# Performance work log

Hardware: AMD Instinct MI355X
Metric: run time of the kernel (lower is better)

## Reference

```python
import jax, jax.numpy as jnp
import numpy as np

B = 2048
GIN = 128      # gating input features
GH = 128       # gating hidden units
E = 8          # experts
XIN = 512      # expert input features
U = 512        # expert layer units
OUT = 512      # expert output features


def setup_inputs() -> dict:
    key = jax.random.key(0)
    ks = jax.random.split(key, 16)
    rn = lambda k, shape: (jax.random.normal(k, shape) * 0.05).astype(jnp.float32)
    return {
        "gating_input": jax.random.normal(ks[0], (B, GIN), dtype=jnp.float32),
        "expert_input": jax.random.normal(ks[1], (B, XIN), dtype=jnp.float32),
        # gating MLP params (Dense stores kernel as (in, out))
        "Wg0": rn(ks[2], (GIN, GH)), "bg0": rn(ks[3], (GH,)),
        "Wg1": rn(ks[4], (GH, GH)), "bg1": rn(ks[5], (GH,)),
        "Wgo": rn(ks[6], (GH, E)),  "bgo": rn(ks[7], (E,)),
        # expert weight pools: alpha (E, units, in), beta (E, units)
        "alpha0": rn(ks[8], (E, U, XIN)), "beta0": rn(ks[9], (E, U)),
        "alpha1": rn(ks[10], (E, U, U)),  "beta1": rn(ks[11], (E, U)),
        "alpha2": rn(ks[12], (E, OUT, U)), "beta2": rn(ks[13], (E, OUT)),
    }


def dense_expert(x, g, alpha, beta):
    # Mathematically: (sum_e g[b,e] * alpha[e]) @ x[b] + sum_e g[b,e]*beta[e]
    # Contract input with each expert first (avoids the (B,U,I) blended-weight tensor).
    per_expert = jnp.einsum("bi,eui->beu", x, alpha)   # (B, E, U)
    w = jnp.einsum("be,beu->bu", g, per_expert)         # (B, U)
    b = jnp.einsum("be,eu->bu", g, beta)                # (B, U)
    return w + b


def reference(gating_input, expert_input, Wg0, bg0, Wg1, bg1, Wgo, bgo,
              alpha0, beta0, alpha1, beta1, alpha2, beta2):
    # Gating network: Dense+ELU x2 (dropout is identity at inference), Dense+softmax
    h = jax.nn.elu(gating_input @ Wg0 + bg0)
    h = jax.nn.elu(h @ Wg1 + bg1)
    g = jax.nn.softmax(h @ Wgo + bgo, axis=-1)          # (B, E)

    # Expert network: DenseExpert + ELU x2, final DenseExpert
    x = jax.nn.elu(dense_expert(expert_input, g, alpha0, beta0))
    x = jax.nn.elu(dense_expert(x, g, alpha1, beta1))
    y = dense_expert(x, g, alpha2, beta2)               # (B, OUT)
    return y
```

## Files before the change

kernel.cpp:

```cpp
#include <hip/hip_runtime.h>
#include <math.h>

#define BATCH 2048
#define GIN 128
#define GH 128
#define NE 8
#define XIN 512
#define UU 512
#define NPAIR 4

typedef __attribute__((ext_vector_type(8))) short short8;
typedef __attribute__((ext_vector_type(4))) float f32x4;

__device__ inline unsigned short f2bf(float f) {
    unsigned u = __float_as_uint(f);
    u += 0x7fffu + ((u >> 16) & 1u);
    return (unsigned short)(u >> 16);
}

__device__ inline float elu1(float x) { return x > 0.f ? x : (expf(x) - 1.f); }

__global__ __launch_bounds__(256) void gating_kernel(
    const float* __restrict__ gin, const float* __restrict__ W0, const float* __restrict__ b0,
    const float* __restrict__ W1, const float* __restrict__ b1,
    const float* __restrict__ Wo, const float* __restrict__ bo,
    float* __restrict__ g)
{
    __shared__ float xs[4][128];
    __shared__ float hs[4][128];
    __shared__ float ps[2][4][128];
    __shared__ float lp[8][4][8];
    __shared__ float ls[4][8];

    const int t = threadIdx.x;
    const int c = t & 127;
    const int h = t >> 7;
    const int row0 = blockIdx.x * 4;

    ((float*)xs)[t]       = gin[row0 * GIN + t];
    ((float*)xs)[t + 256] = gin[row0 * GIN + t + 256];
    __syncthreads();

    {
        float acc0 = 0.f, acc1 = 0.f, acc2 = 0.f, acc3 = 0.f;
        const float* Wc = W0 + c;
        #pragma unroll 8
        for (int i = h * 64; i < h * 64 + 64; ++i) {
            float w = Wc[i * GH];
            acc0 += xs[0][i] * w; acc1 += xs[1][i] * w;
            acc2 += xs[2][i] * w; acc3 += xs[3][i] * w;
        }
        ps[h][0][c] = acc0; ps[h][1][c] = acc1; ps[h][2][c] = acc2; ps[h][3][c] = acc3;
    }
    __syncthreads();
    {
        int o = t, r = o >> 7, cc = o & 127;
        hs[r][cc] = elu1(ps[0][r][cc] + ps[1][r][cc] + b0[cc]);
        o = t + 256; r = o >> 7; cc = o & 127;
        hs[r][cc] = elu1(ps[0][r][cc] + ps[1][r][cc] + b0[cc]);
    }
    __syncthreads();

    {
        float acc0 = 0.f, acc1 = 0.f, acc2 = 0.f, acc3 = 0.f;
        const float* Wc = W1 + c;
        #pragma unroll 8
        for (int i = h * 64; i < h * 64 + 64; ++i) {
            float w = Wc[i * GH];
            acc0 += hs[0][i] * w; acc1 += hs[1][i] * w;
            acc2 += hs[2][i] * w; acc3 += hs[3][i] * w;
        }
        ps[h][0][c] = acc0; ps[h][1][c] = acc1; ps[h][2][c] = acc2; ps[h][3][c] = acc3;
    }
    __syncthreads();
    {
        int o = t, r = o >> 7, cc = o & 127;
        xs[r][cc] = elu1(ps[0][r][cc] + ps[1][r][cc] + b1[cc]);
        o = t + 256; r = o >> 7; cc = o & 127;
        xs[r][cc] = elu1(ps[0][r][cc] + ps[1][r][cc] + b1[cc]);
    }
    __syncthreads();

    {
        const int e = t & 7, r = (t >> 3) & 3, q = t >> 5;
        float s = 0.f;
        #pragma unroll
        for (int i = q * 16; i < q * 16 + 16; ++i) s += xs[r][i] * Wo[i * NE + e];
        lp[q][r][e] = s;
    }
    __syncthreads();
    if (t < 32) {
        const int r = t >> 3, e = t & 7;
        float s = bo[e];
        #pragma unroll
        for (int q = 0; q < 8; ++q) s += lp[q][r][e];
        ls[r][e] = s;
    }
    __syncthreads();
    if (t < 4) {
        float mx = ls[t][0];
        #pragma unroll
        for (int e = 1; e < 8; ++e) mx = fmaxf(mx, ls[t][e]);
        float s = 0.f, ex[8];
        #pragma unroll
        for (int e = 0; e < 8; ++e) { ex[e] = expf(ls[t][e] - mx); s += ex[e]; }
        float inv = 1.f / s;
        #pragma unroll
        for (int e = 0; e < 8; ++e) g[(row0 + t) * NE + e] = ex[e] * inv;
    }
}

__global__ __launch_bounds__(256) void convert_alpha_kernel(
    const float* __restrict__ a0, const float* __restrict__ a1, const float* __restrict__ a2,
    unsigned short* __restrict__ ab)
{
    const long long vi = (long long)(blockIdx.x * blockDim.x + threadIdx.x) * 4;
    const int a = (int)(vi >> 21);
    const int off = (int)(vi & ((1 << 21) - 1));
    const float* src = (a == 0) ? a0 : ((a == 1) ? a1 : a2);
    float4 v = *(const float4*)(src + off);
    union { unsigned short us[4]; uint2 u2; } p;
    p.us[0] = f2bf(v.x); p.us[1] = f2bf(v.y); p.us[2] = f2bf(v.z); p.us[3] = f2bf(v.w);
    *(uint2*)(ab + vi) = p.u2;
}

__global__ __launch_bounds__(256) void xcast_kernel(
    const float* __restrict__ x, unsigned short* __restrict__ Xb)
{
    const int gid4 = (blockIdx.x * blockDim.x + threadIdx.x) * 4;
    const float4 v = *(const float4*)(x + gid4);
    union { unsigned short us[4]; uint2 u2; } p;
    p.us[0] = f2bf(v.x); p.us[1] = f2bf(v.y); p.us[2] = f2bf(v.z); p.us[3] = f2bf(v.w);
    *(uint2*)(Xb + gid4) = p.u2;
}

__global__ __launch_bounds__(256) void moe_gemm_kernel(
    const unsigned short* __restrict__ A,
    const unsigned short* __restrict__ Bw,
    const float* __restrict__ g,
    float* __restrict__ Cp)
{
    constexpr int M = BATCH, N = UU, K = XIN;
    __shared__ unsigned short As[128 * 64];
    __shared__ unsigned short Bs0[64 * 64];
    __shared__ unsigned short Bs1[64 * 64];
    __shared__ float gs[128][2];

    const int t = threadIdx.x;
    const int n0 = blockIdx.x * 64;
    const int m0 = blockIdx.y * 128;
    const int z = blockIdx.z;
    const int e0 = 2 * z, e1 = 2 * z + 1;
    const int wave = t >> 6, lane = t & 63;
    const int wm = (wave >> 1) * 64;
    const int wn = (wave & 1) * 32;

    if (t < 128) {
        gs[t][0] = g[(m0 + t) * NE + e0];
        gs[t][1] = g[(m0 + t) * NE + e1];
    }

    f32x4 acc0[4][2] = {};
    f32x4 acc1[4][2] = {};

    const int trow = t >> 3;
    const int tcol = (t & 7) * 8;

    const unsigned short* Ae  = A  + (size_t)m0 * K;
    const unsigned short* Be0 = Bw + ((size_t)e0 * N + n0) * K;
    const unsigned short* Be1 = Bw + ((size_t)e1 * N + n0) * K;

    for (int ki = 0; ki < K; ki += 64) {
        __syncthreads();
        #pragma unroll
        for (int it = 0; it < 4; ++it) {
            const unsigned short* ga = Ae + (size_t)(trow + it * 32) * K + ki + tcol;
            __builtin_amdgcn_global_load_lds(
                (const __attribute__((address_space(1))) void*)ga,
                (__attribute__((address_space(3))) void*)(As + it * 2048 + t * 8), 16, 0, 0);
        }
        #pragma unroll
        for (int it = 0; it < 2; ++it) {
            const unsigned short* gb0 = Be0 + (size_t)(trow + it * 32) * K + ki + tcol;
            __builtin_amdgcn_global_load_lds(
                (const __attribute__((address_space(1))) void*)gb0,
                (__attribute__((address_space(3))) void*)(Bs0 + it * 2048 + t * 8), 16, 0, 0);
            const unsigned short* gb1 = Be1 + (size_t)(trow + it * 32) * K + ki + tcol;
            __builtin_amdgcn_global_load_lds(
                (const __attribute__((address_space(1))) void*)gb1,
                (__attribute__((address_space(3))) void*)(Bs1 + it * 2048 + t * 8), 16, 0, 0);
        }
        __syncthreads();

        #pragma unroll
        for (int kk = 0; kk < 64; kk += 32) {
            short8 af[4], bf0[2], bf1[2];
            const int fr = lane & 15;
            const int fk = kk + (lane >> 4) * 8;
            #pragma unroll
            for (int i = 0; i < 4; ++i) af[i] = *(const short8*)(As + (wm + fr + i * 16) * 64 + fk);
            #pragma unroll
            for (int j = 0; j < 2; ++j) {
                bf0[j] = *(const short8*)(Bs0 + (wn + fr + j * 16) * 64 + fk);
                bf1[j] = *(const short8*)(Bs1 + (wn + fr + j * 16) * 64 + fk);
            }
            #pragma unroll
            for (int i = 0; i < 4; ++i)
                #pragma unroll
                for (int j = 0; j < 2; ++j) {
                    acc0[i][j] = __builtin_amdgcn_mfma_f32_16x16x32_bf16(af[i], bf0[j], acc0[i][j], 0, 0, 0);
                    acc1[i][j] = __builtin_amdgcn_mfma_f32_16x16x32_bf16(af[i], bf1[j], acc1[i][j], 0, 0, 0);
                }
        }
    }

    float* Cb = Cp + (size_t)z * M * N;
    const int cl = lane & 15, rq = lane >> 4;
    #pragma unroll
    for (int i = 0; i < 4; ++i)
        #pragma unroll
        for (int j = 0; j < 2; ++j)
            #pragma unroll
            for (int r = 0; r < 4; ++r) {
                const int rl = wm + i * 16 + rq * 4 + r;
                const int col = n0 + wn + j * 16 + cl;
                const float v = gs[rl][0] * acc0[i][j][r] + gs[rl][1] * acc1[i][j][r];
                Cb[(size_t)(m0 + rl) * N + col] = v;
            }
}

__global__ __launch_bounds__(256) void reduce_kernel(
    const float* __restrict__ Cp, const float* __restrict__ g,
    const float* __restrict__ beta, unsigned short* __restrict__ Xnext,
    float* __restrict__ out, int last)
{
    const int gid4 = (blockIdx.x * blockDim.x + threadIdx.x) * 4;
    const int b = gid4 >> 9, u = gid4 & 511;
    float4 v = {0.f, 0.f, 0.f, 0.f};
    #pragma unroll
    for (int s = 0; s < NPAIR; ++s) {
        float4 p = *(const float4*)(Cp + (size_t)s * (BATCH * (size_t)UU) + gid4);
        v.x += p.x; v.y += p.y; v.z += p.z; v.w += p.w;
    }
    const float* gb = g + b * NE;
    #pragma unroll
    for (int e = 0; e < NE; ++e) {
        const float ge = gb[e];
        float4 bb = *(const float4*)(beta + e * UU + u);
        v.x += ge * bb.x; v.y += ge * bb.y; v.z += ge * bb.z; v.w += ge * bb.w;
    }
    if (last) {
        *(float4*)(out + gid4) = v;
    } else {
        union { unsigned short us[4]; uint2 u2; } p;
        p.us[0] = f2bf(elu1(v.x)); p.us[1] = f2bf(elu1(v.y));
        p.us[2] = f2bf(elu1(v.z)); p.us[3] = f2bf(elu1(v.w));
        *(uint2*)(Xnext + gid4) = p.u2;
    }
}

extern "C" void kernel_launch(void* const* d_in, const int* in_sizes, int n_in,
                              void* d_out, int out_size, void* d_ws, size_t ws_size,
                              hipStream_t stream)
{
    (void)in_sizes; (void)n_in; (void)out_size; (void)ws_size;
    const float* gin = (const float*)d_in[0];
    const float* xin = (const float*)d_in[1];
    const float* W0  = (const float*)d_in[2];
    const float* b0  = (const float*)d_in[3];
    const float* W1  = (const float*)d_in[4];
    const float* b1  = (const float*)d_in[5];
    const float* Wo  = (const float*)d_in[6];
    const float* bo  = (const float*)d_in[7];
    const float* alpha[3] = {(const float*)d_in[8],  (const float*)d_in[10], (const float*)d_in[12]};
    const float* beta[3]  = {(const float*)d_in[9],  (const float*)d_in[11], (const float*)d_in[13]};
    float* out = (float*)d_out;

    char* ws = (char*)d_ws;
    float* g = (float*)ws;
    size_t off = 65536;
    unsigned short* ab = (unsigned short*)(ws + off);
    off += (size_t)3 * (1 << 21) * 2;
    unsigned short* Xb = (unsigned short*)(ws + off);
    off += (size_t)BATCH * XIN * 2;
    float* Cp = (float*)(ws + off);

    gating_kernel<<<BATCH / 4, 256, 0, stream>>>(gin, W0, b0, W1, b1, Wo, bo, g);
    convert_alpha_kernel<<<(3 * (1 << 21)) / 4 / 256, 256, 0, stream>>>(alpha[0], alpha[1], alpha[2], ab);
    xcast_kernel<<<(BATCH * XIN) / 4 / 256, 256, 0, stream>>>(xin, Xb);

    for (int l = 0; l < 3; ++l) {
        moe_gemm_kernel<<<dim3(UU / 64, BATCH / 128, NPAIR), 256, 0, stream>>>(
            Xb, ab + (size_t)l * (1 << 21), g, Cp);
        reduce_kernel<<<(BATCH * UU) / 4 / 256, 256, 0, stream>>>(
            Cp, g, beta[l], Xb, out, l == 2 ? 1 : 0);
    }
}
```

Baseline: 183.4 us.

## Fuse all-expert GEMM with gating reduction, bias and ELU epilogue

Each block now computes a 64x32 output tile for all 8 experts at once and folds gating weights, the bias mix and ELU into the epilogue. This removes the fp32 partial-sum buffer and the separate reduce kernel per layer. Ping-pong activation buffers are used, and the x cast is merged into the alpha conversion launch. The cost is more accumulator registers (16 f32x4 per wave), a smaller A tile with less reuse, and non-coalesced scalar stores in the epilogue.

Result: faster. 157.4 us (-14.2%).

```diff
diff --git a/kernel.cpp b/kernel.cpp
--- a/kernel.cpp
+++ b/kernel.cpp
@@ -7,7 +7,6 @@
 #define NE 8
 #define XIN 512
 #define UU 512
-#define NPAIR 4
 
 typedef __attribute__((ext_vector_type(8))) short short8;
 typedef __attribute__((ext_vector_type(4))) float f32x4;
@@ -110,153 +109,102 @@
     }
 }
 
-__global__ __launch_bounds__(256) void convert_alpha_kernel(
+__global__ __launch_bounds__(256) void convert_kernel(
     const float* __restrict__ a0, const float* __restrict__ a1, const float* __restrict__ a2,
-    unsigned short* __restrict__ ab)
+    const float* __restrict__ xv, unsigned short* __restrict__ dst)
 {
     const long long vi = (long long)(blockIdx.x * blockDim.x + threadIdx.x) * 4;
-    const int a = (int)(vi >> 21);
-    const int off = (int)(vi & ((1 << 21) - 1));
-    const float* src = (a == 0) ? a0 : ((a == 1) ? a1 : a2);
-    float4 v = *(const float4*)(src + off);
+    const int sel = (int)(vi >> 21);
+    const float* src = (sel == 0) ? a0 : (sel == 1) ? a1 : (sel == 2) ? a2 : xv;
+    float4 v = *(const float4*)(src + (vi & ((1 << 21) - 1)));
     union { unsigned short us[4]; uint2 u2; } p;
     p.us[0] = f2bf(v.x); p.us[1] = f2bf(v.y); p.us[2] = f2bf(v.z); p.us[3] = f2bf(v.w);
-    *(uint2*)(ab + vi) = p.u2;
-}
-
-__global__ __launch_bounds__(256) void xcast_kernel(
-    const float* __restrict__ x, unsigned short* __restrict__ Xb)
-{
-    const int gid4 = (blockIdx.x * blockDim.x + threadIdx.x) * 4;
-    const float4 v = *(const float4*)(x + gid4);
-    union { unsigned short us[4]; uint2 u2; } p;
-    p.us[0] = f2bf(v.x); p.us[1] = f2bf(v.y); p.us[2] = f2bf(v.z); p.us[3] = f2bf(v.w);
-    *(uint2*)(Xb + gid4) = p.u2;
-}
-
-__global__ __launch_bounds__(256) void moe_gemm_kernel(
+    *(uint2*)(dst + vi) = p.u2;
+}
+
+__global__ __launch_bounds__(256) void moe_fused_kernel(
     const unsigned short* __restrict__ A,
     const unsigned short* __restrict__ Bw,
     const float* __restrict__ g,
-    float* __restrict__ Cp)
-{
-    constexpr int M = BATCH, N = UU, K = XIN;
-    __shared__ unsigned short As[128 * 64];
-    __shared__ unsigned short Bs0[64 * 64];
-    __shared__ unsigned short Bs1[64 * 64];
-    __shared__ float gs[128][2];
+    const float* __restrict__ beta,
+    unsigned short* __restrict__ Xnext,
+    float* __restrict__ out, int last)
+{
+    constexpr int K = XIN;
+    __shared__ unsigned short As[64 * 64];
+    __shared__ unsigned short Bs[8 * 32 * 64];
+    __shared__ float gs[64][8];
+    __shared__ float bt[8][32];
 
     const int t = threadIdx.x;
-    const int n0 = blockIdx.x * 64;
-    const int m0 = blockIdx.y * 128;
-    const int z = blockIdx.z;
-    const int e0 = 2 * z, e1 = 2 * z + 1;
+    const int n0 = blockIdx.x * 32;
+    const int m0 = blockIdx.y * 64;
     const int wave = t >> 6, lane = t & 63;
-    const int wm = (wave >> 1) * 64;
-    const int wn = (wave & 1) * 32;
-
-    if (t < 128) {
-        gs[t][0] = g[(m0 + t) * NE + e0];
-        gs[t][1] = g[(m0 + t) * NE + e1];
-    }
-
-    f32x4 acc0[4][2] = {};
-    f32x4 acc1[4][2] = {};
+    const int wm = (wave >> 1) * 32;
+    const int wn = (wave & 1) * 16;
+
+    ((float2*)gs)[t] = ((const float2*)(g + (size_t)m0 * NE))[t];
+    bt[t >> 5][t & 31] = beta[(t >> 5) * UU + n0 + (t & 31)];
+
+    f32x4 acc[8][2] = {};
 
     const int trow = t >> 3;
     const int tcol = (t & 7) * 8;
 
-    const unsigned short* Ae  = A  + (size_t)m0 * K;
-    const unsigned short* Be0 = Bw + ((size_t)e0 * N + n0) * K;
-    const unsigned short* Be1 = Bw + ((size_t)e1 * N + n0) * K;
+    const unsigned short* Ae = A + (size_t)m0 * K;
 
     for (int ki = 0; ki < K; ki += 64) {
         __syncthreads();
         #pragma unroll
-        for (int it = 0; it < 4; ++it) {
+        for (int it = 0; it < 2; ++it) {
             const unsigned short* ga = Ae + (size_t)(trow + it * 32) * K + ki + tcol;
             __builtin_amdgcn_global_load_lds(
                 (const __attribute__((address_space(1))) void*)ga,
                 (__attribute__((address_space(3))) void*)(As + it * 2048 + t * 8), 16, 0, 0);
         }
         #pragma unroll
-        for (int it = 0; it < 2; ++it) {
-            const unsigned short* gb0 = Be0 + (size_t)(trow + it * 32) * K + ki + tcol;
+        for (int it = 0; it < 8; ++it) {
+            const int rowflat = trow + it * 32;
+            const unsigned short* gb = Bw +
+                ((size_t)(rowflat >> 5) * UU + n0 + (rowflat & 31)) * K + ki + tcol;
             __builtin_amdgcn_global_load_lds(
-                (const __attribute__((address_space(1))) void*)gb0,
-                (__attribute__((address_space(3))) void*)(Bs0 + it * 2048 + t * 8), 16, 0, 0);
-            const unsigned short* gb1 = Be1 + (size_t)(trow + it * 32) * K + ki + tcol;
-            __builtin_amdgcn_global_load_lds(
-                (const __attribute__((address_space(1))) void*)gb1,
-                (__attribute__((address_space(3))) void*)(Bs1 + it * 2048 + t * 8), 16, 0, 0);
+                (const __attribute__((address_space(1))) void*)gb,
+                (__attribute__((address_space(3))) void*)(Bs + it * 2048 + t * 8), 16, 0, 0);
         }
         __syncthreads();
 
         #pragma unroll
         for (int kk = 0; kk < 64; kk += 32) {
-            short8 af[4], bf0[2], bf1[2];
+            short8 af[2], bf[8];
             const int fr = lane & 15;
             const int fk = kk + (lane >> 4) * 8;
+            af[0] = *(const short8*)(As + (wm + fr) * 64 + fk);
+            af[1] = *(const short8*)(As + (wm + fr + 16) * 64 + fk);
             #pragma unroll
-            for (int i = 0; i < 4; ++i) af[i] = *(const short8*)(As + (wm + fr + i * 16) * 64 + fk);
+            for (int e = 0; e < 8; ++e)
+                bf[e] = *(const short8*)(Bs + (e * 32 + wn + fr) * 64 + fk);
             #pragma unroll
-            for (int j = 0; j < 2; ++j) {
-                bf0[j] = *(const short8*)(Bs0 + (wn + fr + j * 16) * 64 + fk);
-                bf1[j] = *(const short8*)(Bs1 + (wn + fr + j * 16) * 64 + fk);
+            for (int e = 0; e < 8; ++e) {
+                acc[e][0] = __builtin_amdgcn_mfma_f32_16x16x32_bf16(af[0], bf[e], acc[e][0], 0, 0, 0);
+                acc[e][1] = __builtin_amdgcn_mfma_f32_16x16x32_bf16(af[1], bf[e], acc[e][1], 0, 0, 0);
             }
+        }
+    }
+
+    const int cl = lane & 15, rq = lane >> 4;
+    const int col = n0 + wn + cl;
+    #pragma unroll
+    for (int i = 0; i < 2; ++i)
+        #pragma unroll
+        for (int r = 0; r < 4; ++r) {
+            const int rl = wm + i * 16 + rq * 4 + r;
+            float v = 0.f;
             #pragma unroll
-            for (int i = 0; i < 4; ++i)
-                #pragma unroll
-                for (int j = 0; j < 2; ++j) {
-                    acc0[i][j] = __builtin_amdgcn_mfma_f32_16x16x32_bf16(af[i], bf0[j], acc0[i][j], 0, 0, 0);
-                    acc1[i][j] = __builtin_amdgcn_mfma_f32_16x16x32_bf16(af[i], bf1[j], acc1[i][j], 0, 0, 0);
-                }
-        }
-    }
-
-    float* Cb = Cp + (size_t)z * M * N;
-    const int cl = lane & 15, rq = lane >> 4;
-    #pragma unroll
-    for (int i = 0; i < 4; ++i)
-        #pragma unroll
-        for (int j = 0; j < 2; ++j)
-            #pragma unroll
-            for (int r = 0; r < 4; ++r) {
-                const int rl = wm + i * 16 + rq * 4 + r;
-                const int col = n0 + wn + j * 16 + cl;
-                const float v = gs[rl][0] * acc0[i][j][r] + gs[rl][1] * acc1[i][j][r];
-                Cb[(size_t)(m0 + rl) * N + col] = v;
-            }
-}
-
-__global__ __launch_bounds__(256) void reduce_kernel(
-    const float* __restrict__ Cp, const float* __restrict__ g,
-    const float* __restrict__ beta, unsigned short* __restrict__ Xnext,
-    float* __restrict__ out, int last)
-{
-    const int gid4 = (blockIdx.x * blockDim.x + threadIdx.x) * 4;
-    const int b = gid4 >> 9, u = gid4 & 511;
-    float4 v = {0.f, 0.f, 0.f, 0.f};
-    #pragma unroll
-    for (int s = 0; s < NPAIR; ++s) {
-        float4 p = *(const float4*)(Cp + (size_t)s * (BATCH * (size_t)UU) + gid4);
-        v.x += p.x; v.y += p.y; v.z += p.z; v.w += p.w;
-    }
-    const float* gb = g + b * NE;
-    #pragma unroll
-    for (int e = 0; e < NE; ++e) {
-        const float ge = gb[e];
-        float4 bb = *(const float4*)(beta + e * UU + u);
-        v.x += ge * bb.x; v.y += ge * bb.y; v.z += ge * bb.z; v.w += ge * bb.w;
-    }
-    if (last) {
-        *(float4*)(out + gid4) = v;
-    } else {
-        union { unsigned short us[4]; uint2 u2; } p;
-        p.us[0] = f2bf(elu1(v.x)); p.us[1] = f2bf(elu1(v.y));
-        p.us[2] = f2bf(elu1(v.z)); p.us[3] = f2bf(elu1(v.w));
-        *(uint2*)(Xnext + gid4) = p.u2;
-    }
+            for (int e = 0; e < 8; ++e)
+                v += gs[rl][e] * (acc[e][i][r] + bt[e][wn + cl]);
+            if (last) out[(size_t)(m0 + rl) * UU + col] = v;
+            else      Xnext[(size_t)(m0 + rl) * UU + col] = f2bf(elu1(v));
+        }
 }
 
 extern "C" void kernel_launch(void* const* d_in, const int* in_sizes, int n_in,
@@ -281,18 +229,20 @@
     size_t off = 65536;
     unsigned short* ab = (unsigned short*)(ws + off);
     off += (size_t)3 * (1 << 21) * 2;
-    unsigned short* Xb = (unsigned short*)(ws + off);
+    unsigned short* Xb0 = (unsigned short*)(ws + off);
     off += (size_t)BATCH * XIN * 2;
-    float* Cp = (float*)(ws + off);
+    unsigned short* Xb1 = (unsigned short*)(ws + off);
+    off += (size_t)BATCH * XIN * 2;
 
     gating_kernel<<<BATCH / 4, 256, 0, stream>>>(gin, W0, b0, W1, b1, Wo, bo, g);
-    convert_alpha_kernel<<<(3 * (1 << 21)) / 4 / 256, 256, 0, stream>>>(alpha[0], alpha[1], alpha[2], ab);
-    xcast_kernel<<<(BATCH * XIN) / 4 / 256, 256, 0, stream>>>(xin, Xb);
-
+    convert_kernel<<<(3 * (1 << 21) + BATCH * XIN) / 4 / 256, 256, 0, stream>>>(
+        alpha[0], alpha[1], alpha[2], xin, ab);
+
+    unsigned short* Xsrc = Xb0;
+    unsigned short* Xdst = Xb1;
     for (int l = 0; l < 3; ++l) {
-        moe_gemm_kernel<<<dim3(UU / 64, BATCH / 128, NPAIR), 256, 0, stream>>>(
-            Xb, ab + (size_t)l * (1 << 21), g, Cp);
-        reduce_kernel<<<(BATCH * UU) / 4 / 256, 256, 0, stream>>>(
-            Cp, g, beta[l], Xb, out, l == 2 ? 1 : 0);
-    }
-}
+        moe_fused_kernel<<<dim3(UU / 32, BATCH / 64), 256, 0, stream>>>(
+            Xsrc, ab + (size_t)l * (1 << 21), g, beta[l], Xdst, out, l == 2 ? 1 : 0);
+        unsigned short* tmp = Xsrc; Xsrc = Xdst; Xdst = tmp;
+    }
+}
```
